# Optimization experiments

Hardware: AMD Instinct MI355X
Metric: run time of the kernel (lower is better)

The kernel has to match this reference:

```python
import jax, jax.numpy as jnp
import numpy as np


def setup_inputs() -> dict:
    key = jax.random.key(0)
    kq, kk, kv = jax.random.split(key, 3)
    B, H, S, D = 4, 16, 2048, 64
    q = jax.random.normal(kq, (B, H, S, D), dtype=jnp.float32)
    k = jax.random.normal(kk, (B, H, S, D), dtype=jnp.float32)
    v = jax.random.normal(kv, (B, H, S, D), dtype=jnp.float32)
    return {"q": q, "k": k, "v": v}


def reference(q, k, v):
    # scale = sqrt(d_k); source's self.scale is undefined, standard SDPA scaling assumed
    scale = jnp.asarray(np.sqrt(q.shape[-1]), dtype=q.dtype)
    # [B,H,S,S] scores; sigmoid instead of softmax (no normalization across keys)
    scores = jnp.einsum("bhqd,bhkd->bhqk", q, k) / scale
    attn = jax.nn.sigmoid(scores)
    return jnp.einsum("bhqk,bhkd->bhqd", attn, v)
```

## Files before the change

### kernel.cpp

```cpp
#include <hip/hip_runtime.h>


typedef __bf16 bf16_t;
typedef __attribute__((ext_vector_type(8))) __bf16 bf16x8;
typedef __attribute__((ext_vector_type(4))) __bf16 bf16x4;
typedef __attribute__((ext_vector_type(4))) float  f32x4;
typedef __attribute__((ext_vector_type(4))) short  short4v;

#if defined(__HIP_DEVICE_COMPILE__) && __has_builtin(__builtin_amdgcn_exp2f)
#define FAST_EXP2(x) __builtin_amdgcn_exp2f(x)
#else
#define FAST_EXP2(x) exp2f(x)
#endif
#if defined(__HIP_DEVICE_COMPILE__) && __has_builtin(__builtin_amdgcn_rcpf)
#define FAST_RCP(x) __builtin_amdgcn_rcpf(x)
#else
#define FAST_RCP(x) (1.0f / (x))
#endif

static __device__ __forceinline__ f32x4 pv_mfma(bf16x4 a, bf16x4 b, f32x4 c) {
#if defined(__HIP_DEVICE_COMPILE__)
#if __has_builtin(__builtin_amdgcn_mfma_f32_16x16x16_bf16)
    return __builtin_amdgcn_mfma_f32_16x16x16_bf16(a, b, c, 0, 0, 0);
#elif __has_builtin(__builtin_amdgcn_mfma_f32_16x16x16bf16_1k)
    return __builtin_amdgcn_mfma_f32_16x16x16bf16_1k(
        __builtin_bit_cast(short4v, a), __builtin_bit_cast(short4v, b), c, 0, 0, 0);
#else
    f32x4 d;
    asm("v_mfma_f32_16x16x16_bf16 %0, %1, %2, %3"
        : "=v"(d) : "v"(a), "v"(b), "v"(c));
    return d;
#endif
#else
    (void)a; (void)b;
    return c;
#endif
}

static constexpr int SEQ = 2048;
static constexpr int DH  = 64;
static constexpr int KB  = 32;
static constexpr int NIT = SEQ / KB;
static constexpr int QPW = 32;
static constexpr int QPB = 128;

__global__ __launch_bounds__(256, 4)
void sigattn_kernel(const float* __restrict__ Qg, const float* __restrict__ Kg,
                    const float* __restrict__ Vg, float* __restrict__ Og)
{
    __shared__ bf16_t Kbuf[2][4 * 64 * 8];
    __shared__ bf16_t Vbuf[2][4 * 64 * 8];

    const int t    = threadIdx.x;
    const int wave = t >> 6;
    const int lane = t & 63;
    const int c16  = lane & 15;
    const int g4   = lane >> 4;

    const int bh    = blockIdx.x;
    const int qtile = blockIdx.y;

    const size_t hbase = (size_t)bh * SEQ * DH;
    const float* Qp = Qg + hbase;
    const float* Kp = Kg + hbase;
    const float* Vp = Vg + hbase;
    float*       Op = Og + hbase;

    const int qwave = qtile * QPB + wave * QPW;

    const float qscale = -0.125f * 1.44269504088896340736f;
    bf16x8 qf[2][2];
    #pragma unroll
    for (int qs = 0; qs < 2; ++qs) {
        #pragma unroll
        for (int dh = 0; dh < 2; ++dh) {
            const float* p = Qp + (size_t)(qwave + qs * 16 + c16) * DH + dh * 32 + g4 * 8;
            f32x4 a = *(const f32x4*)p;
            f32x4 b = *(const f32x4*)(p + 4);
            bf16x8 f;
            f[0] = (bf16_t)(a.x * qscale); f[1] = (bf16_t)(a.y * qscale);
            f[2] = (bf16_t)(a.z * qscale); f[3] = (bf16_t)(a.w * qscale);
            f[4] = (bf16_t)(b.x * qscale); f[5] = (bf16_t)(b.y * qscale);
            f[6] = (bf16_t)(b.z * qscale); f[7] = (bf16_t)(b.w * qscale);
            qf[qs][dh] = f;
        }
    }

    f32x4 kst0, kst1;
    float vst[8];
    auto issue_loads = [&](int kb0) {
        const float* pk = Kp + (size_t)(kb0 + (wave >> 1) * 16 + c16) * DH + (wave & 1) * 32 + g4 * 8;
        kst0 = *(const f32x4*)pk;
        kst1 = *(const f32x4*)(pk + 4);
        const float* pv = Vp + (size_t)(kb0 + g4 * 4) * DH + wave * 16 + c16;
        #pragma unroll
        for (int h = 0; h < 2; ++h)
            #pragma unroll
            for (int j = 0; j < 4; ++j)
                vst[h * 4 + j] = pv[(size_t)(h * 16 + j) * DH];
    };
    auto store_lds = [&](int buf) {
        bf16x8 k8;
        k8[0] = (bf16_t)kst0.x; k8[1] = (bf16_t)kst0.y; k8[2] = (bf16_t)kst0.z; k8[3] = (bf16_t)kst0.w;
        k8[4] = (bf16_t)kst1.x; k8[5] = (bf16_t)kst1.y; k8[6] = (bf16_t)kst1.z; k8[7] = (bf16_t)kst1.w;
        *(bf16x8*)&Kbuf[buf][t * 8] = k8;
        bf16x8 v8;
        #pragma unroll
        for (int j = 0; j < 8; ++j) v8[j] = (bf16_t)vst[j];
        *(bf16x8*)&Vbuf[buf][t * 8] = v8;
    };

    issue_loads(0);
    store_lds(0);

    f32x4 acc[2][4] = {};

    for (int it = 0; it < NIT; ++it) {
        const int buf = it & 1;
        __syncthreads();
        if (it + 1 < NIT) issue_loads((it + 1) * KB);

        bf16x8 kf[4], vf[4];
        #pragma unroll
        for (int f = 0; f < 4; ++f) kf[f] = *(const bf16x8*)&Kbuf[buf][(f * 64 + lane) * 8];
        #pragma unroll
        for (int f = 0; f < 4; ++f) vf[f] = *(const bf16x8*)&Vbuf[buf][(f * 64 + lane) * 8];

        #pragma unroll
        for (int qs = 0; qs < 2; ++qs) {
            #pragma unroll
            for (int ks = 0; ks < 2; ++ks) {
                f32x4 s = {0.f, 0.f, 0.f, 0.f};
                s = __builtin_amdgcn_mfma_f32_16x16x32_bf16(kf[ks * 2 + 0], qf[qs][0], s, 0, 0, 0);
                s = __builtin_amdgcn_mfma_f32_16x16x32_bf16(kf[ks * 2 + 1], qf[qs][1], s, 0, 0, 0);
                bf16x4 p;
                #pragma unroll
                for (int r = 0; r < 4; ++r)
                    p[r] = (bf16_t)FAST_RCP(1.0f + FAST_EXP2(s[r]));
                #pragma unroll
                for (int dt = 0; dt < 4; ++dt) {
                    bf16x4 vb = ks == 0
                        ? __builtin_shufflevector(vf[dt], vf[dt], 0, 1, 2, 3)
                        : __builtin_shufflevector(vf[dt], vf[dt], 4, 5, 6, 7);
                    acc[qs][dt] = pv_mfma(p, vb, acc[qs][dt]);
                }
            }
        }

        if (it + 1 < NIT) store_lds(buf ^ 1);
    }

    #pragma unroll
    for (int qs = 0; qs < 2; ++qs) {
        const int q0 = qwave + qs * 16 + g4 * 4;
        #pragma unroll
        for (int r = 0; r < 4; ++r) {
            float* po = Op + (size_t)(q0 + r) * DH + c16;
            po[0]  = acc[qs][0][r];
            po[16] = acc[qs][1][r];
            po[32] = acc[qs][2][r];
            po[48] = acc[qs][3][r];
        }
    }
}

extern "C" void kernel_launch(void* const* d_in, const int* in_sizes, int n_in,
                              void* d_out, int out_size, void* d_ws, size_t ws_size,
                              hipStream_t stream)
{
    const float* q = (const float*)d_in[0];
    const float* k = (const float*)d_in[1];
    const float* v = (const float*)d_in[2];
    float* o = (float*)d_out;
    dim3 grid(64, SEQ / QPB);
    sigattn_kernel<<<grid, dim3(256), 0, stream>>>(q, k, v, o);
}
```

Measured before the change: 216.5 us.

## Pre-convert K/V to bf16 MFMA layout in workspace and use 16x16x32 PV MFMA

Adds a prepass kernel that converts K and V from fp32 to bf16 once per head and writes them to the workspace already in the per-tile LDS layout. The main kernel then streams contiguous bf16 chunks into LDS with no conversion and no strided V gathers. This removes the repeated fp32 loads and casts that every query tile paid for each key block. The PV product also switches from two 16x16x16 MFMAs per key half to one 16x16x32 MFMA over both halves. The costs are an extra launch and a workspace round trip, with the old path kept as a fallback when the workspace is too small.

```diff
diff --git a/kernel.cpp b/kernel.cpp
--- a/kernel.cpp
+++ b/kernel.cpp
@@ -5,7 +5,6 @@
 typedef __attribute__((ext_vector_type(8))) __bf16 bf16x8;
 typedef __attribute__((ext_vector_type(4))) __bf16 bf16x4;
 typedef __attribute__((ext_vector_type(4))) float  f32x4;
-typedef __attribute__((ext_vector_type(4))) short  short4v;
 
 #if defined(__HIP_DEVICE_COMPILE__) && __has_builtin(__builtin_amdgcn_exp2f)
 #define FAST_EXP2(x) __builtin_amdgcn_exp2f(x)
@@ -15,27 +14,8 @@
 #if defined(__HIP_DEVICE_COMPILE__) && __has_builtin(__builtin_amdgcn_rcpf)
 #define FAST_RCP(x) __builtin_amdgcn_rcpf(x)
 #else
-#define FAST_RCP(x) (1.0f / (x))
+#define FAST_RCP(x) (1.0f/(x))
 #endif
-
-static __device__ __forceinline__ f32x4 pv_mfma(bf16x4 a, bf16x4 b, f32x4 c) {
-#if defined(__HIP_DEVICE_COMPILE__)
-#if __has_builtin(__builtin_amdgcn_mfma_f32_16x16x16_bf16)
-    return __builtin_amdgcn_mfma_f32_16x16x16_bf16(a, b, c, 0, 0, 0);
-#elif __has_builtin(__builtin_amdgcn_mfma_f32_16x16x16bf16_1k)
-    return __builtin_amdgcn_mfma_f32_16x16x16bf16_1k(
-        __builtin_bit_cast(short4v, a), __builtin_bit_cast(short4v, b), c, 0, 0, 0);
-#else
-    f32x4 d;
-    asm("v_mfma_f32_16x16x16_bf16 %0, %1, %2, %3"
-        : "=v"(d) : "v"(a), "v"(b), "v"(c));
-    return d;
-#endif
-#else
-    (void)a; (void)b;
-    return c;
-#endif
-}
 
 static constexpr int SEQ = 2048;
 static constexpr int DH  = 64;
@@ -43,13 +23,52 @@
 static constexpr int NIT = SEQ / KB;
 static constexpr int QPW = 32;
 static constexpr int QPB = 128;
+static constexpr int CHUNK = 4096;
+
+__global__ __launch_bounds__(256)
+void sigattn_prepass(const float* __restrict__ Kg, const float* __restrict__ Vg,
+                     bf16_t* __restrict__ ws)
+{
+    const int bh = blockIdx.x, it = blockIdx.y;
+    const int t  = threadIdx.x;
+    const int kb = it * KB;
+    const size_t hbase = (size_t)bh * SEQ * DH;
+    bf16_t* wbase = ws + ((size_t)bh * NIT + it) * CHUNK;
+
+    {
+        const int f = t >> 6, lane = t & 63;
+        const int ks = f >> 1, dh = f & 1, c16 = lane & 15, g4 = lane >> 4;
+        const float* p = Kg + hbase + (size_t)(kb + ks * 16 + c16) * DH + dh * 32 + g4 * 8;
+        f32x4 a = *(const f32x4*)p;
+        f32x4 b = *(const f32x4*)(p + 4);
+        bf16x8 o;
+        o[0] = (bf16_t)a.x; o[1] = (bf16_t)a.y; o[2] = (bf16_t)a.z; o[3] = (bf16_t)a.w;
+        o[4] = (bf16_t)b.x; o[5] = (bf16_t)b.y; o[6] = (bf16_t)b.z; o[7] = (bf16_t)b.w;
+        *(bf16x8*)&wbase[(size_t)t * 8] = o;
+    }
+    {
+        const int c = t & 63, rblk = t >> 6;
+        const int dt = c >> 4, c16 = c & 15;
+        const float* p = Vg + hbase + (size_t)(kb + rblk * 8) * DH + c;
+        float v[8];
+        #pragma unroll
+        for (int i = 0; i < 8; ++i) v[i] = p[(size_t)i * DH];
+        const int j0  = (rblk >> 1) * 4;
+        const int g4a = (rblk & 1) * 2;
+        bf16x4 ca, cb;
+        #pragma unroll
+        for (int i = 0; i < 4; ++i) { ca[i] = (bf16_t)v[i]; cb[i] = (bf16_t)v[4 + i]; }
+        bf16_t* vr = wbase + 2048;
+        *(bf16x4*)&vr[(size_t)(dt * 64 + g4a * 16 + c16) * 8 + j0]       = ca;
+        *(bf16x4*)&vr[(size_t)(dt * 64 + (g4a + 1) * 16 + c16) * 8 + j0] = cb;
+    }
+}
 
 __global__ __launch_bounds__(256, 4)
-void sigattn_kernel(const float* __restrict__ Qg, const float* __restrict__ Kg,
-                    const float* __restrict__ Vg, float* __restrict__ Og)
-{
-    __shared__ bf16_t Kbuf[2][4 * 64 * 8];
-    __shared__ bf16_t Vbuf[2][4 * 64 * 8];
+void sigattn_main(const float* __restrict__ Qg, const bf16_t* __restrict__ ws,
+                  float* __restrict__ Og)
+{
+    __shared__ __align__(16) bf16_t buf[2][CHUNK];
 
     const int t    = threadIdx.x;
     const int wave = t >> 6;
@@ -60,11 +79,9 @@
     const int bh    = blockIdx.x;
     const int qtile = blockIdx.y;
 
-    const size_t hbase = (size_t)bh * SEQ * DH;
-    const float* Qp = Qg + hbase;
-    const float* Kp = Kg + hbase;
-    const float* Vp = Vg + hbase;
-    float*       Op = Og + hbase;
+    const float* Qp = Qg + (size_t)bh * SEQ * DH;
+    float*       Op = Og + (size_t)bh * SEQ * DH;
+    const bf16_t* wsh = ws + (size_t)bh * NIT * CHUNK;
 
     const int qwave = qtile * QPB + wave * QPW;
 
@@ -86,68 +103,51 @@
         }
     }
 
-    f32x4 kst0, kst1;
-    float vst[8];
-    auto issue_loads = [&](int kb0) {
-        const float* pk = Kp + (size_t)(kb0 + (wave >> 1) * 16 + c16) * DH + (wave & 1) * 32 + g4 * 8;
-        kst0 = *(const f32x4*)pk;
-        kst1 = *(const f32x4*)(pk + 4);
-        const float* pv = Vp + (size_t)(kb0 + g4 * 4) * DH + wave * 16 + c16;
-        #pragma unroll
-        for (int h = 0; h < 2; ++h)
-            #pragma unroll
-            for (int j = 0; j < 4; ++j)
-                vst[h * 4 + j] = pv[(size_t)(h * 16 + j) * DH];
-    };
-    auto store_lds = [&](int buf) {
-        bf16x8 k8;
-        k8[0] = (bf16_t)kst0.x; k8[1] = (bf16_t)kst0.y; k8[2] = (bf16_t)kst0.z; k8[3] = (bf16_t)kst0.w;
-        k8[4] = (bf16_t)kst1.x; k8[5] = (bf16_t)kst1.y; k8[6] = (bf16_t)kst1.z; k8[7] = (bf16_t)kst1.w;
-        *(bf16x8*)&Kbuf[buf][t * 8] = k8;
-        bf16x8 v8;
-        #pragma unroll
-        for (int j = 0; j < 8; ++j) v8[j] = (bf16_t)vst[j];
-        *(bf16x8*)&Vbuf[buf][t * 8] = v8;
-    };
-
-    issue_loads(0);
-    store_lds(0);
+    bf16x8 rK, rV;
+    auto gload = [&](int it) {
+        const bf16_t* g = wsh + (size_t)it * CHUNK + t * 8;
+        rK = *(const bf16x8*)g;
+        rV = *(const bf16x8*)(g + 2048);
+    };
+    auto lstore = [&](int nb) {
+        *(bf16x8*)&buf[nb][t * 8]        = rK;
+        *(bf16x8*)&buf[nb][2048 + t * 8] = rV;
+    };
+
+    gload(0);
+    lstore(0);
 
     f32x4 acc[2][4] = {};
 
     for (int it = 0; it < NIT; ++it) {
-        const int buf = it & 1;
+        const int cur = it & 1;
         __syncthreads();
-        if (it + 1 < NIT) issue_loads((it + 1) * KB);
+        if (it + 1 < NIT) gload(it + 1);
 
         bf16x8 kf[4], vf[4];
         #pragma unroll
-        for (int f = 0; f < 4; ++f) kf[f] = *(const bf16x8*)&Kbuf[buf][(f * 64 + lane) * 8];
-        #pragma unroll
-        for (int f = 0; f < 4; ++f) vf[f] = *(const bf16x8*)&Vbuf[buf][(f * 64 + lane) * 8];
+        for (int f = 0; f < 4; ++f) kf[f] = *(const bf16x8*)&buf[cur][(f * 64 + lane) * 8];
+        #pragma unroll
+        for (int f = 0; f < 4; ++f) vf[f] = *(const bf16x8*)&buf[cur][2048 + (f * 64 + lane) * 8];
 
         #pragma unroll
         for (int qs = 0; qs < 2; ++qs) {
-            #pragma unroll
-            for (int ks = 0; ks < 2; ++ks) {
-                f32x4 s = {0.f, 0.f, 0.f, 0.f};
-                s = __builtin_amdgcn_mfma_f32_16x16x32_bf16(kf[ks * 2 + 0], qf[qs][0], s, 0, 0, 0);
-                s = __builtin_amdgcn_mfma_f32_16x16x32_bf16(kf[ks * 2 + 1], qf[qs][1], s, 0, 0, 0);
-                bf16x4 p;
-                #pragma unroll
-                for (int r = 0; r < 4; ++r)
-                    p[r] = (bf16_t)FAST_RCP(1.0f + FAST_EXP2(s[r]));
-                #pragma unroll
-                for (int dt = 0; dt < 4; ++dt) {
-                    bf16x4 vb = ks == 0
-                        ? __builtin_shufflevector(vf[dt], vf[dt], 0, 1, 2, 3)
-                        : __builtin_shufflevector(vf[dt], vf[dt], 4, 5, 6, 7);
-                    acc[qs][dt] = pv_mfma(p, vb, acc[qs][dt]);
-                }
-            }
-        }
-
-        if (it + 1 < NIT) store_lds(buf ^ 1);
+            f32x4 s0 = {0.f, 0.f, 0.f, 0.f}, s1 = {0.f, 0.f, 0.f, 0.f};
+            s0 = __builtin_amdgcn_mfma_f32_16x16x32_bf16(kf[0], qf[qs][0], s0, 0, 0, 0);
+            s0 = __builtin_amdgcn_mfma_f32_16x16x32_bf16(kf[1], qf[qs][1], s0, 0, 0, 0);
+            s1 = __builtin_amdgcn_mfma_f32_16x16x32_bf16(kf[2], qf[qs][0], s1, 0, 0, 0);
+            s1 = __builtin_amdgcn_mfma_f32_16x16x32_bf16(kf[3], qf[qs][1], s1, 0, 0, 0);
+            bf16x8 p8;
+            #pragma unroll
+            for (int r = 0; r < 4; ++r) p8[r]     = (bf16_t)FAST_RCP(1.0f + FAST_EXP2(s0[r]));
+            #pragma unroll
+            for (int r = 0; r < 4; ++r) p8[4 + r] = (bf16_t)FAST_RCP(1.0f + FAST_EXP2(s1[r]));
+            #pragma unroll
+            for (int dt = 0; dt < 4; ++dt)
+                acc[qs][dt] = __builtin_amdgcn_mfma_f32_16x16x32_bf16(p8, vf[dt], acc[qs][dt], 0, 0, 0);
+        }
+
+        if (it + 1 < NIT) lstore(cur ^ 1);
     }
 
     #pragma unroll
@@ -164,6 +164,95 @@
     }
 }
 
+__global__ __launch_bounds__(256, 4)
+void sigattn_fallback(const float* __restrict__ Qg, const float* __restrict__ Kg,
+                      const float* __restrict__ Vg, float* __restrict__ Og)
+{
+    __shared__ bf16_t Kbuf[2][4 * 64 * 8];
+    __shared__ bf16_t Vbuf[2][4 * 64 * 8];
+    const int t = threadIdx.x, wave = t >> 6, lane = t & 63;
+    const int c16 = lane & 15, g4 = lane >> 4;
+    const int bh = blockIdx.x, qtile = blockIdx.y;
+    const size_t hbase = (size_t)bh * SEQ * DH;
+    const float* Qp = Qg + hbase; const float* Kp = Kg + hbase;
+    const float* Vp = Vg + hbase; float* Op = Og + hbase;
+    const int qwave = qtile * QPB + wave * QPW;
+    const float qscale = -0.125f * 1.44269504088896340736f;
+    bf16x8 qf[2][2];
+    #pragma unroll
+    for (int qs = 0; qs < 2; ++qs)
+        #pragma unroll
+        for (int dh = 0; dh < 2; ++dh) {
+            const float* p = Qp + (size_t)(qwave + qs * 16 + c16) * DH + dh * 32 + g4 * 8;
+            f32x4 a = *(const f32x4*)p; f32x4 b = *(const f32x4*)(p + 4);
+            bf16x8 f;
+            f[0]=(bf16_t)(a.x*qscale); f[1]=(bf16_t)(a.y*qscale); f[2]=(bf16_t)(a.z*qscale); f[3]=(bf16_t)(a.w*qscale);
+            f[4]=(bf16_t)(b.x*qscale); f[5]=(bf16_t)(b.y*qscale); f[6]=(bf16_t)(b.z*qscale); f[7]=(bf16_t)(b.w*qscale);
+            qf[qs][dh] = f;
+        }
+    f32x4 kst0, kst1; float vst[8];
+    auto issue_loads = [&](int kb0) {
+        const float* pk = Kp + (size_t)(kb0 + (wave >> 1) * 16 + c16) * DH + (wave & 1) * 32 + g4 * 8;
+        kst0 = *(const f32x4*)pk; kst1 = *(const f32x4*)(pk + 4);
+        const float* pv = Vp + (size_t)(kb0 + g4 * 4) * DH + wave * 16 + c16;
+        #pragma unroll
+        for (int h = 0; h < 2; ++h)
+            #pragma unroll
+            for (int j = 0; j < 4; ++j) vst[h * 4 + j] = pv[(size_t)(h * 16 + j) * DH];
+    };
+    auto store_lds = [&](int buf) {
+        bf16x8 k8;
+        k8[0]=(bf16_t)kst0.x; k8[1]=(bf16_t)kst0.y; k8[2]=(bf16_t)kst0.z; k8[3]=(bf16_t)kst0.w;
+        k8[4]=(bf16_t)kst1.x; k8[5]=(bf16_t)kst1.y; k8[6]=(bf16_t)kst1.z; k8[7]=(bf16_t)kst1.w;
+        *(bf16x8*)&Kbuf[buf][t * 8] = k8;
+        bf16x8 v8;
+        #pragma unroll
+        for (int j = 0; j < 8; ++j) v8[j] = (bf16_t)vst[j];
+        *(bf16x8*)&Vbuf[buf][t * 8] = v8;
+    };
+    issue_loads(0); store_lds(0);
+    f32x4 acc[2][4] = {};
+    for (int it = 0; it < NIT; ++it) {
+        const int buf = it & 1;
+        __syncthreads();
+        if (it + 1 < NIT) issue_loads((it + 1) * KB);
+        bf16x8 kf[4], vf[4];
+        #pragma unroll
+        for (int f = 0; f < 4; ++f) kf[f] = *(const bf16x8*)&Kbuf[buf][(f * 64 + lane) * 8];
+        #pragma unroll
+        for (int f = 0; f < 4; ++f) vf[f] = *(const bf16x8*)&Vbuf[buf][(f * 64 + lane) * 8];
+        #pragma unroll
+        for (int qs = 0; qs < 2; ++qs) {
+            f32x4 s0 = {0.f,0.f,0.f,0.f}, s1 = {0.f,0.f,0.f,0.f};
+            s0 = __builtin_amdgcn_mfma_f32_16x16x32_bf16(kf[0], qf[qs][0], s0, 0, 0, 0);
+            s0 = __builtin_amdgcn_mfma_f32_16x16x32_bf16(kf[1], qf[qs][1], s0, 0, 0, 0);
+            s1 = __builtin_amdgcn_mfma_f32_16x16x32_bf16(kf[2], qf[qs][0], s1, 0, 0, 0);
+            s1 = __builtin_amdgcn_mfma_f32_16x16x32_bf16(kf[3], qf[qs][1], s1, 0, 0, 0);
+            bf16x8 p8;
+            #pragma unroll
+            for (int r = 0; r < 4; ++r) p8[r]     = (bf16_t)FAST_RCP(1.0f + FAST_EXP2(s0[r]));
+            #pragma unroll
+            for (int r = 0; r < 4; ++r) p8[4 + r] = (bf16_t)FAST_RCP(1.0f + FAST_EXP2(s1[r]));
+            #pragma unroll
+            for (int dt = 0; dt < 4; ++dt)
+                acc[qs][dt] = __builtin_amdgcn_mfma_f32_16x16x32_bf16(p8, vf[dt], acc[qs][dt], 0, 0, 0);
+        }
+        if (it + 1 < NIT) store_lds(buf ^ 1);
+    }
+    #pragma unroll
+    for (int qs = 0; qs < 2; ++qs) {
+        const int q0 = qwave + qs * 16 + g4 * 4;
+        #pragma unroll
+        for (int r = 0; r < 4; ++r) {
+            float* po = Op + (size_t)(q0 + r) * DH + c16;
+            po[0]  = acc[qs][0][r];
+            po[16] = acc[qs][1][r];
+            po[32] = acc[qs][2][r];
+            po[48] = acc[qs][3][r];
+        }
+    }
+}
+
 extern "C" void kernel_launch(void* const* d_in, const int* in_sizes, int n_in,
                               void* d_out, int out_size, void* d_ws, size_t ws_size,
                               hipStream_t stream)
@@ -172,6 +261,11 @@
     const float* k = (const float*)d_in[1];
     const float* v = (const float*)d_in[2];
     float* o = (float*)d_out;
-    dim3 grid(64, SEQ / QPB);
-    sigattn_kernel<<<grid, dim3(256), 0, stream>>>(q, k, v, o);
-}
+    const size_t need = 64ull * NIT * CHUNK * sizeof(bf16_t);
+    if (ws_size >= need) {
+        sigattn_prepass<<<dim3(64, NIT), dim3(256), 0, stream>>>(k, v, (bf16_t*)d_ws);
+        sigattn_main<<<dim3(64, SEQ / QPB), dim3(256), 0, stream>>>(q, (const bf16_t*)d_ws, o);
+    } else {
+        sigattn_fallback<<<dim3(64, SEQ / QPB), dim3(256), 0, stream>>>(q, k, v, o);
+    }
+}
```

Result: faster. 202.0 us (-6.7%).
